# Kernel tuning notes

Measured on AMD Instinct MI355X. Metric: run time of the kernel, lower is better.

The kernel has to match this reference:

```python
import jax, jax.numpy as jnp
import numpy as np

B, N, D = 4, 2048, 1024  # in_features == out_features required by the original code path
SPARSITY = 0.01


def setup_inputs() -> dict:
    key = jax.random.key(0)
    k1, k2, k3 = jax.random.split(key, 3)
    x = jax.random.normal(k1, (B, N, D), dtype=jnp.float32)
    # Reproduce FrequencyLinearLayer.__init__: sparse top-k frequency weights.
    spatial = jax.random.normal(k2, (D, D), dtype=jnp.float32) * 0.02
    freq = jnp.fft.fft(spatial, axis=-1)  # complex64, (out, in) consumed as (D_in, D_out)
    k = int(D * SPARSITY)
    mag = jnp.abs(freq)
    kth = jax.lax.top_k(mag, k)[0][:, -1:]  # k-th largest magnitude per row
    w_sparse = jnp.where(mag >= kth, freq, 0.0 + 0.0j)
    bias = jax.random.normal(k3, (D,), dtype=jnp.float32) * 0.01
    return {
        "x": x,
        "w_freq_real": jnp.real(w_sparse).astype(jnp.float32),
        "w_freq_imag": jnp.imag(w_sparse).astype(jnp.float32),
        "bias": bias,
    }


def reference(x, w_freq_real, w_freq_imag, bias):
    # y = real(IFFT(FFT(x) @ W_freq)) + bias
    # The original materializes a (B,N,D_in,D_out) complex intermediate via
    # unsqueeze*multiply -> sum; that is exactly a complex matmul, expressed here as einsum.
    w = jax.lax.complex(w_freq_real, w_freq_imag)            # (D_in, D_out) complex64
    x_freq = jnp.fft.fft(x, axis=-1)                          # (B, N, D_in) complex64
    y_freq = jnp.einsum('bnd,do->bno', x_freq, w)             # (B, N, D_out)
    y = jnp.real(jnp.fft.ifft(y_freq, axis=-1))               # (B, N, D_out) float32
    return y + bias
```

## Files before the change

### kernel.cpp

```cpp
#include <hip/hip_runtime.h>
#include <hip/hip_bf16.h>
#include <math.h>

#define DD 1024
#define BT 8192
#define TWO_PI 6.28318530717958647692f

typedef float f32x4 __attribute__((ext_vector_type(4)));
typedef short bf16x8 __attribute__((ext_vector_type(8)));
typedef unsigned short u16x8 __attribute__((ext_vector_type(8)));
typedef unsigned short u16x4 __attribute__((ext_vector_type(4)));
typedef const __attribute__((address_space(1))) void g_void;
typedef __attribute__((address_space(3))) void l_void;

__device__ __forceinline__ unsigned short f2bf(float f) {
  unsigned int u = __float_as_uint(f);
  unsigned int r = (u + 0x7FFFu + ((u >> 16) & 1u)) >> 16;
  return (unsigned short)r;
}

__global__ __launch_bounds__(256) void transpose_W_kernel(
    const float* __restrict__ Wr, const float* __restrict__ Wi,
    float2* __restrict__ Wt) {
  __shared__ float tr[64][65];
  __shared__ float ti[64][65];
  const int k0 = blockIdx.y * 64, o0 = blockIdx.x * 64;
  for (int q = threadIdx.x; q < 64 * 64; q += 256) {
    int r = q >> 6, c = q & 63;
    tr[r][c] = Wr[(size_t)(k0 + r) * DD + o0 + c];
    ti[r][c] = Wi[(size_t)(k0 + r) * DD + o0 + c];
  }
  __syncthreads();
  for (int q = threadIdx.x; q < 64 * 64; q += 256) {
    int r = q >> 6, c = q & 63;
    Wt[(size_t)(o0 + r) * DD + k0 + c] = make_float2(tr[c][r], ti[c][r]);
  }
}

__global__ __launch_bounds__(256) void build_T_kernel(
    const float2* __restrict__ Wt, float2* __restrict__ T) {
  __shared__ float2 tw[DD];
  __shared__ int    kidx[DD];
  __shared__ float2 wval[DD];
  __shared__ int    offs[257];
  const int o = blockIdx.x, tid = threadIdx.x;

  for (int j = tid; j < DD; j += 256) {
    float s, c;
    sincosf((TWO_PI / DD) * (float)j, &s, &c);
    tw[j] = make_float2(c, s);
  }
  int cnt = 0;
  for (int k = tid; k < DD; k += 256) {
    float2 w = Wt[(size_t)o * DD + k];
    if (w.x != 0.f || w.y != 0.f) cnt++;
  }
  offs[tid + 1] = cnt;
  __syncthreads();
  if (tid == 0) {
    offs[0] = 0;
    for (int i = 1; i <= 256; i++) offs[i] += offs[i - 1];
  }
  __syncthreads();
  int p = offs[tid];
  for (int k = tid; k < DD; k += 256) {
    float2 w = Wt[(size_t)o * DD + k];
    if (w.x != 0.f || w.y != 0.f) { kidx[p] = k; wval[p] = w; p++; }
  }
  __syncthreads();
  const int nnz = offs[256];
  for (int d = tid; d < DD; d += 256) {
    float re = 0.f, im = 0.f;
    for (int j = 0; j < nnz; j++) {
      int    k  = kidx[j];
      float2 w  = wval[j];
      float2 cs = tw[(k * d) & (DD - 1)];
      re += w.x * cs.x + w.y * cs.y;
      im += w.y * cs.x - w.x * cs.y;
    }
    T[(size_t)o * DD + d] = make_float2(re, im);
  }
}

__global__ __launch_bounds__(256) void transpose_T_kernel(
    const float2* __restrict__ T, unsigned short* __restrict__ TT) {
  __shared__ float2 tile[64][65];
  const int o0 = blockIdx.x * 64, d0 = blockIdx.y * 64;
  for (int q = threadIdx.x; q < 64 * 64; q += 256) {
    int r = q >> 6, c = q & 63;
    tile[r][c] = T[(size_t)(o0 + r) * DD + d0 + c];
  }
  __syncthreads();
  for (int q = threadIdx.x; q < 64 * 64; q += 256) {
    int r = q >> 6, c = q & 63;
    float2 v = tile[c][r];
    TT[(size_t)(d0 + r) * 2048 + o0 + c]        = f2bf(v.x);
    TT[(size_t)(d0 + r) * 2048 + 1024 + o0 + c] = f2bf(v.y);
  }
}

__global__ __launch_bounds__(256) void gen_CS_kernel(unsigned short* __restrict__ CS) {
  int idx = blockIdx.x * 256 + threadIdx.x;
  int m = idx >> 10, o = idx & 1023;
  float s, c;
  sincosf((TWO_PI / DD) * (float)((m * o) & (DD - 1)), &s, &c);
  CS[(size_t)m * 2048 + o]        = f2bf(c);
  CS[(size_t)m * 2048 + 1024 + o] = f2bf(-s);
}

__global__ __launch_bounds__(256) void convert_x_kernel(
    const float* __restrict__ X, unsigned short* __restrict__ Xb) {
  size_t i = (size_t)blockIdx.x * 256 + threadIdx.x;
  const float4* p = (const float4*)(X + i * 8);
  float4 a = p[0], b = p[1];
  u16x8 v;
  v[0] = f2bf(a.x); v[1] = f2bf(a.y); v[2] = f2bf(a.z); v[3] = f2bf(a.w);
  v[4] = f2bf(b.x); v[5] = f2bf(b.y); v[6] = f2bf(b.z); v[7] = f2bf(b.w);
  *(u16x8*)(Xb + i * 8) = v;
}

template <int LDK, int MODE>
__global__ __launch_bounds__(256) void mfma_nt_kernel(
    const unsigned short* __restrict__ A,
    const unsigned short* __restrict__ B,
    const float* __restrict__ bias,
    float* __restrict__ Out, float scale, int ldo, int kLen) {
  __shared__ __align__(16) unsigned short Asm[128 * 32];
  __shared__ __align__(16) unsigned short Bsm[128 * 32];
  const int tid  = threadIdx.x;
  const int wave = tid >> 6, lane = tid & 63;
  const int wr = wave >> 1, wc = wave & 1;
  const int row0 = blockIdx.y * 128;
  const int col0 = blockIdx.x * 128;
  const int kBeg = blockIdx.z * kLen;

  f32x4 acc[4][4] = {};

  for (int k0 = kBeg; k0 < kBeg + kLen; k0 += 32) {
    __syncthreads();
#pragma unroll
    for (int is = 0; is < 2; is++) {
      int e = is * 256 + tid;
      int r = e >> 2, c = (e & 3) * 8;
      const unsigned short* ga = A + (size_t)(row0 + r) * LDK + k0 + c;
      const unsigned short* gb = B + (size_t)(col0 + r) * LDK + k0 + c;
      __builtin_amdgcn_global_load_lds((g_void*)ga, (l_void*)(Asm + is * 2048 + wave * 512), 16, 0, 0);
      __builtin_amdgcn_global_load_lds((g_void*)gb, (l_void*)(Bsm + is * 2048 + wave * 512), 16, 0, 0);
    }
    __syncthreads();

    bf16x8 af[4], bfr[4];
#pragma unroll
    for (int i = 0; i < 4; i++) {
      int ra = wr * 64 + i * 16 + (lane & 15);
      af[i]  = *(const bf16x8*)&Asm[ra * 32 + (lane >> 4) * 8];
      int rb = wc * 64 + i * 16 + (lane & 15);
      bfr[i] = *(const bf16x8*)&Bsm[rb * 32 + (lane >> 4) * 8];
    }
#pragma unroll
    for (int i = 0; i < 4; i++)
#pragma unroll
      for (int j = 0; j < 4; j++)
        acc[i][j] = __builtin_amdgcn_mfma_f32_16x16x32_bf16(af[i], bfr[j], acc[i][j], 0, 0, 0);
  }

  const int crow0 = row0 + wr * 64;
  const int ccol0 = col0 + wc * 64;
  if (MODE == 2) {
    float* O = Out + (size_t)blockIdx.z * DD * DD;
#pragma unroll
    for (int i = 0; i < 4; i++)
#pragma unroll
      for (int j = 0; j < 4; j++) {
        int cc = ccol0 + j * 16 + (lane & 15);
#pragma unroll
        for (int v = 0; v < 4; v++) {
          int rr = crow0 + i * 16 + (lane >> 4) * 4 + v;
          O[(size_t)rr * ldo + cc] = acc[i][j][v];
        }
      }
  } else {
    float bv[4];
#pragma unroll
    for (int j = 0; j < 4; j++)
      bv[j] = bias[ccol0 + j * 16 + (lane & 15)];
#pragma unroll
    for (int i = 0; i < 4; i++)
#pragma unroll
      for (int j = 0; j < 4; j++) {
        int cc = ccol0 + j * 16 + (lane & 15);
#pragma unroll
        for (int v = 0; v < 4; v++) {
          int rr = crow0 + i * 16 + (lane >> 4) * 4 + v;
          Out[(size_t)rr * ldo + cc] = acc[i][j][v] * scale + bv[j];
        }
      }
  }
}

__global__ __launch_bounds__(256) void reduce_M_kernel(
    const float* __restrict__ P, unsigned short* __restrict__ Mb) {
  const size_t NE = (size_t)DD * DD;
  size_t i = ((size_t)blockIdx.x * 256 + threadIdx.x) * 4;
  float4 s = *(const float4*)(P + i);
#pragma unroll
  for (int z = 1; z < 4; z++) {
    float4 p = *(const float4*)(P + z * NE + i);
    s.x += p.x; s.y += p.y; s.z += p.z; s.w += p.w;
  }
  const float inv = 1.0f / (float)DD;
  u16x4 v;
  v[0] = f2bf(s.x * inv); v[1] = f2bf(s.y * inv);
  v[2] = f2bf(s.z * inv); v[3] = f2bf(s.w * inv);
  *(u16x4*)(Mb + i) = v;
}

extern "C" void kernel_launch(void* const* d_in, const int* in_sizes, int n_in,
                              void* d_out, int out_size, void* d_ws, size_t ws_size,
                              hipStream_t stream) {
  const float* x    = (const float*)d_in[0];
  const float* wrp  = (const float*)d_in[1];
  const float* wip  = (const float*)d_in[2];
  const float* bias = (const float*)d_in[3];
  float*       y    = (float*)d_out;

  char* ws = (char*)d_ws;
  const size_t MB = 1024 * 1024;
  float2*         Wt = (float2*)(ws + 0);
  float2*         T  = (float2*)(ws + 8  * MB);
  unsigned short* TT = (unsigned short*)(ws + 16 * MB);
  unsigned short* CS = (unsigned short*)(ws + 20 * MB);
  unsigned short* Mb = (unsigned short*)(ws + 24 * MB);
  float*          P  = (float*)(ws + 0);
  unsigned short* Xb = (unsigned short*)(ws + 0);

  transpose_W_kernel<<<dim3(16, 16), 256, 0, stream>>>(wrp, wip, Wt);
  build_T_kernel<<<DD, 256, 0, stream>>>(Wt, T);
  transpose_T_kernel<<<dim3(16, 16), 256, 0, stream>>>(T, TT);
  gen_CS_kernel<<<4096, 256, 0, stream>>>(CS);
  mfma_nt_kernel<2048, 2><<<dim3(8, 8, 4), 256, 0, stream>>>(
      CS, TT, nullptr, P, 1.0f, DD, 512);
  reduce_M_kernel<<<DD * DD / (256 * 4), 256, 0, stream>>>(P, Mb);
  convert_x_kernel<<<4096, 256, 0, stream>>>(x, Xb);
  mfma_nt_kernel<1024, 0><<<dim3(8, 64, 1), 256, 0, stream>>>(
      Xb, Mb, bias, y, 1.0f, DD, 1024);
}
```

Measured before the change: 99.48 us.

## Deepen GEMM K-step, remap blocks across XCDs, parallelize sparse-index scan

The GEMM kernel now loads two 32-wide K slices per barrier pair, halving the number of synchronizations per tile, and uses a 1D grid with a swizzle that spreads consecutive tiles over the eight XCDs for better L2 locality. build_T replaces the serial single-thread prefix sum and double global read with register-held nonzeros and a parallel Hillis-Steele scan, shrinking shared index buffers to 64 entries. LDS use per GEMM block doubles, and the scan assumes at most 4 nonzeros per thread and 64 per row.

Result: slower. 106.6 us (+7.2%).

```diff
diff --git a/kernel.cpp b/kernel.cpp
--- a/kernel.cpp
+++ b/kernel.cpp
@@ -40,9 +40,9 @@
 __global__ __launch_bounds__(256) void build_T_kernel(
     const float2* __restrict__ Wt, float2* __restrict__ T) {
   __shared__ float2 tw[DD];
-  __shared__ int    kidx[DD];
-  __shared__ float2 wval[DD];
-  __shared__ int    offs[257];
+  __shared__ int    kidx[64];
+  __shared__ float2 wval[64];
+  __shared__ int    sc[256];
   const int o = blockIdx.x, tid = threadIdx.x;
 
   for (int j = tid; j < DD; j += 256) {
@@ -51,24 +51,27 @@
     tw[j] = make_float2(c, s);
   }
   int cnt = 0;
-  for (int k = tid; k < DD; k += 256) {
+  float2 wl[4];
+  int    kl[4];
+#pragma unroll
+  for (int q = 0; q < 4; q++) {
+    int k = tid + q * 256;
     float2 w = Wt[(size_t)o * DD + k];
-    if (w.x != 0.f || w.y != 0.f) cnt++;
-  }
-  offs[tid + 1] = cnt;
-  __syncthreads();
-  if (tid == 0) {
-    offs[0] = 0;
-    for (int i = 1; i <= 256; i++) offs[i] += offs[i - 1];
-  }
-  __syncthreads();
-  int p = offs[tid];
-  for (int k = tid; k < DD; k += 256) {
-    float2 w = Wt[(size_t)o * DD + k];
-    if (w.x != 0.f || w.y != 0.f) { kidx[p] = k; wval[p] = w; p++; }
-  }
-  __syncthreads();
-  const int nnz = offs[256];
+    if (w.x != 0.f || w.y != 0.f) { wl[cnt] = w; kl[cnt] = k; cnt++; }
+  }
+  sc[tid] = cnt;
+  __syncthreads();
+#pragma unroll
+  for (int dstep = 1; dstep < 256; dstep <<= 1) {
+    int v = (tid >= dstep) ? sc[tid - dstep] : 0;
+    __syncthreads();
+    sc[tid] += v;
+    __syncthreads();
+  }
+  int p = sc[tid] - cnt;
+  for (int q = 0; q < cnt; q++) { kidx[p + q] = kl[q]; wval[p + q] = wl[q]; }
+  __syncthreads();
+  const int nnz = sc[255];
   for (int d = tid; d < DD; d += 256) {
     float re = 0.f, im = 0.f;
     for (int j = 0; j < nnz; j++) {
@@ -119,55 +122,70 @@
   *(u16x8*)(Xb + i * 8) = v;
 }
 
-template <int LDK, int MODE>
+template <int LDK, int MODE, int GX>
 __global__ __launch_bounds__(256) void mfma_nt_kernel(
     const unsigned short* __restrict__ A,
     const unsigned short* __restrict__ B,
     const float* __restrict__ bias,
     float* __restrict__ Out, float scale, int ldo, int kLen) {
-  __shared__ __align__(16) unsigned short Asm[128 * 32];
-  __shared__ __align__(16) unsigned short Bsm[128 * 32];
+  __shared__ __align__(16) unsigned short Asm[2][128 * 32];
+  __shared__ __align__(16) unsigned short Bsm[2][128 * 32];
   const int tid  = threadIdx.x;
   const int wave = tid >> 6, lane = tid & 63;
   const int wr = wave >> 1, wc = wave & 1;
-  const int row0 = blockIdx.y * 128;
-  const int col0 = blockIdx.x * 128;
-  const int kBeg = blockIdx.z * kLen;
+
+  const int L     = blockIdx.x;
+  const int chunk = gridDim.x >> 3;
+  const int W     = (L & 7) * chunk + (L >> 3);
+  const int tx    = W % GX;
+  const int tyz   = W / GX;
+  const int ty    = (MODE == 2) ? (tyz & 7) : tyz;
+  const int tz    = (MODE == 2) ? (tyz >> 3) : 0;
+
+  const int row0 = ty * 128;
+  const int col0 = tx * 128;
+  const int kBeg = tz * kLen;
 
   f32x4 acc[4][4] = {};
 
-  for (int k0 = kBeg; k0 < kBeg + kLen; k0 += 32) {
-    __syncthreads();
-#pragma unroll
-    for (int is = 0; is < 2; is++) {
-      int e = is * 256 + tid;
-      int r = e >> 2, c = (e & 3) * 8;
-      const unsigned short* ga = A + (size_t)(row0 + r) * LDK + k0 + c;
-      const unsigned short* gb = B + (size_t)(col0 + r) * LDK + k0 + c;
-      __builtin_amdgcn_global_load_lds((g_void*)ga, (l_void*)(Asm + is * 2048 + wave * 512), 16, 0, 0);
-      __builtin_amdgcn_global_load_lds((g_void*)gb, (l_void*)(Bsm + is * 2048 + wave * 512), 16, 0, 0);
+  for (int k0 = kBeg; k0 < kBeg + kLen; k0 += 64) {
+    __syncthreads();
+#pragma unroll
+    for (int h = 0; h < 2; h++) {
+#pragma unroll
+      for (int is = 0; is < 2; is++) {
+        int e = is * 256 + tid;
+        int r = e >> 2, c = (e & 3) * 8;
+        const unsigned short* ga = A + (size_t)(row0 + r) * LDK + k0 + h * 32 + c;
+        const unsigned short* gb = B + (size_t)(col0 + r) * LDK + k0 + h * 32 + c;
+        __builtin_amdgcn_global_load_lds((g_void*)ga, (l_void*)(Asm[h] + is * 2048 + wave * 512), 16, 0, 0);
+        __builtin_amdgcn_global_load_lds((g_void*)gb, (l_void*)(Bsm[h] + is * 2048 + wave * 512), 16, 0, 0);
+      }
     }
     __syncthreads();
 
-    bf16x8 af[4], bfr[4];
-#pragma unroll
-    for (int i = 0; i < 4; i++) {
-      int ra = wr * 64 + i * 16 + (lane & 15);
-      af[i]  = *(const bf16x8*)&Asm[ra * 32 + (lane >> 4) * 8];
-      int rb = wc * 64 + i * 16 + (lane & 15);
-      bfr[i] = *(const bf16x8*)&Bsm[rb * 32 + (lane >> 4) * 8];
+#pragma unroll
+    for (int h = 0; h < 2; h++) {
+      bf16x8 af[4], bfr[4];
+#pragma unroll
+      for (int i = 0; i < 4; i++) {
+        int ra = wr * 64 + i * 16 + (lane & 15);
+        af[i]  = *(const bf16x8*)&Asm[h][ra * 32 + (lane >> 4) * 8];
+        int rb = wc * 64 + i * 16 + (lane & 15);
+        bfr[i] = *(const bf16x8*)&Bsm[h][rb * 32 + (lane >> 4) * 8];
+      }
+#pragma unroll
+      for (int i = 0; i < 4; i++)
+#pragma unroll
+        for (int j = 0; j < 4; j++)
+          acc[i][j] = __builtin_amdgcn_mfma_f32_16x16x32_bf16(af[i], bfr[j], acc[i][j], 0, 0, 0);
     }
-#pragma unroll
-    for (int i = 0; i < 4; i++)
-#pragma unroll
-      for (int j = 0; j < 4; j++)
-        acc[i][j] = __builtin_amdgcn_mfma_f32_16x16x32_bf16(af[i], bfr[j], acc[i][j], 0, 0, 0);
   }
 
   const int crow0 = row0 + wr * 64;
   const int ccol0 = col0 + wc * 64;
   if (MODE == 2) {
-    float* O = Out + (size_t)blockIdx.z * DD * DD;
+    float* O = Out + (size_t)tz * DD * DD;
 #pragma unroll
     for (int i = 0; i < 4; i++)
 #pragma unroll
@@ -238,10 +256,10 @@
   build_T_kernel<<<DD, 256, 0, stream>>>(Wt, T);
   transpose_T_kernel<<<dim3(16, 16), 256, 0, stream>>>(T, TT);
   gen_CS_kernel<<<4096, 256, 0, stream>>>(CS);
-  mfma_nt_kernel<2048, 2><<<dim3(8, 8, 4), 256, 0, stream>>>(
+  mfma_nt_kernel<2048, 2, 8><<<256, 256, 0, stream>>>(
       CS, TT, nullptr, P, 1.0f, DD, 512);
   reduce_M_kernel<<<DD * DD / (256 * 4), 256, 0, stream>>>(P, Mb);
   convert_x_kernel<<<4096, 256, 0, stream>>>(x, Xb);
-  mfma_nt_kernel<1024, 0><<<dim3(8, 64, 1), 256, 0, stream>>>(
+  mfma_nt_kernel<1024, 0, 8><<<512, 256, 0, stream>>>(
       Xb, Mb, bias, y, 1.0f, DD, 1024);
 }
```

## Double-buffer final GEMM with swizzled LDS and parallelize nnz compaction scan

Applied to the files above, without the earlier changes.

The final X·M GEMM is replaced by a dedicated kernel that uses a BK of 64, double-buffers its LDS tiles so the next tile's global loads overlap the current tile's MFMAs, and XOR-swizzles the LDS layout to reduce bank conflicts. build_T's serial single-thread prefix sum becomes a parallel Hillis-Steele scan, and nonzeros are kept in registers so W is read once. The scan assumes at most 4 nonzeros per thread and 64 per row, which holds for 1% sparsity but would overflow for denser weights.

New measurement: 102.0 us. 2.5% more time.

```diff
diff --git a/kernel.cpp b/kernel.cpp
--- a/kernel.cpp
+++ b/kernel.cpp
@@ -40,9 +40,9 @@
 __global__ __launch_bounds__(256) void build_T_kernel(
     const float2* __restrict__ Wt, float2* __restrict__ T) {
   __shared__ float2 tw[DD];
-  __shared__ int    kidx[DD];
-  __shared__ float2 wval[DD];
-  __shared__ int    offs[257];
+  __shared__ int    kidx[64];
+  __shared__ float2 wval[64];
+  __shared__ int    sc[256];
   const int o = blockIdx.x, tid = threadIdx.x;
 
   for (int j = tid; j < DD; j += 256) {
@@ -51,24 +51,27 @@
     tw[j] = make_float2(c, s);
   }
   int cnt = 0;
-  for (int k = tid; k < DD; k += 256) {
+  float2 wl[4];
+  int    kl[4];
+#pragma unroll
+  for (int q = 0; q < 4; q++) {
+    int k = tid + q * 256;
     float2 w = Wt[(size_t)o * DD + k];
-    if (w.x != 0.f || w.y != 0.f) cnt++;
-  }
-  offs[tid + 1] = cnt;
-  __syncthreads();
-  if (tid == 0) {
-    offs[0] = 0;
-    for (int i = 1; i <= 256; i++) offs[i] += offs[i - 1];
-  }
-  __syncthreads();
-  int p = offs[tid];
-  for (int k = tid; k < DD; k += 256) {
-    float2 w = Wt[(size_t)o * DD + k];
-    if (w.x != 0.f || w.y != 0.f) { kidx[p] = k; wval[p] = w; p++; }
-  }
-  __syncthreads();
-  const int nnz = offs[256];
+    if (w.x != 0.f || w.y != 0.f) { wl[cnt] = w; kl[cnt] = k; cnt++; }
+  }
+  sc[tid] = cnt;
+  __syncthreads();
+#pragma unroll
+  for (int dstep = 1; dstep < 256; dstep <<= 1) {
+    int v = (tid >= dstep) ? sc[tid - dstep] : 0;
+    __syncthreads();
+    sc[tid] += v;
+    __syncthreads();
+  }
+  int p = sc[tid] - cnt;
+  for (int q = 0; q < cnt; q++) { kidx[p + q] = kl[q]; wval[p + q] = wl[q]; }
+  __syncthreads();
+  const int nnz = sc[255];
   for (int d = tid; d < DD; d += 256) {
     float re = 0.f, im = 0.f;
     for (int j = 0; j < nnz; j++) {
@@ -215,6 +218,85 @@
   *(u16x4*)(Mb + i) = v;
 }
 
+__global__ __launch_bounds__(256) void gemm_y_kernel(
+    const unsigned short* __restrict__ Xb,
+    const unsigned short* __restrict__ Mb,
+    const float* __restrict__ bias,
+    float* __restrict__ Y) {
+  __shared__ __align__(16) unsigned short Asm[2][128 * 64];
+  __shared__ __align__(16) unsigned short Bsm[2][128 * 64];
+  const int tid  = threadIdx.x;
+  const int wave = tid >> 6, lane = tid & 63;
+  const int wr = wave >> 1, wc = wave & 1;
+  const int row0 = blockIdx.y * 128;
+  const int col0 = blockIdx.x * 128;
+
+#define STAGE(buf, kk)                                                        \
+  {                                                                           \
+    _Pragma("unroll")                                                         \
+    for (int p = 0; p < 4; p++) {                                             \
+      int e  = p * 256 + tid;                                                 \
+      int r  = e >> 3;                                                        \
+      int cs = ((e & 7) ^ ((e >> 3) & 7)) * 8;                                \
+      const unsigned short* ga = Xb + (size_t)(row0 + r) * DD + (kk) + cs;    \
+      const unsigned short* gb = Mb + (size_t)(col0 + r) * DD + (kk) + cs;    \
+      __builtin_amdgcn_global_load_lds((g_void*)ga,                           \
+          (l_void*)(Asm[buf] + p * 2048 + wave * 512), 16, 0, 0);             \
+      __builtin_amdgcn_global_load_lds((g_void*)gb,                           \
+          (l_void*)(Bsm[buf] + p * 2048 + wave * 512), 16, 0, 0);             \
+    }                                                                         \
+  }
+
+  f32x4 acc[4][4] = {};
+
+  STAGE(0, 0);
+  __syncthreads();
+
+  for (int t = 0; t < 16; ++t) {
+    const int cur = t & 1;
+    if (t < 15) STAGE(cur ^ 1, (t + 1) * 64);
+
+#pragma unroll
+    for (int half = 0; half < 2; half++) {
+      bf16x8 af[4], bfr[4];
+#pragma unroll
+      for (int i = 0; i < 4; i++) {
+        int ra = wr * 64 + i * 16 + (lane & 15);
+        int ca = ((half * 4 + (lane >> 4)) ^ (ra & 7)) * 8;
+        af[i]  = *(const bf16x8*)&Asm[cur][ra * 64 + ca];
+        int rb = wc * 64 + i * 16 + (lane & 15);
+        int cb = ((half * 4 + (lane >> 4)) ^ (rb & 7)) * 8;
+        bfr[i] = *(const bf16x8*)&Bsm[cur][rb * 64 + cb];
+      }
+#pragma unroll
+      for (int i = 0; i < 4; i++)
+#pragma unroll
+        for (int j = 0; j < 4; j++)
+          acc[i][j] = __builtin_amdgcn_mfma_f32_16x16x32_bf16(af[i], bfr[j], acc[i][j], 0, 0, 0);
+    }
+    __syncthreads();
+  }
+#undef STAGE
+
+  const int crow0 = row0 + wr * 64;
+  const int ccol0 = col0 + wc * 64;
+  float bv[4];
+#pragma unroll
+  for (int j = 0; j < 4; j++)
+    bv[j] = bias[ccol0 + j * 16 + (lane & 15)];
+#pragma unroll
+  for (int i = 0; i < 4; i++)
+#pragma unroll
+    for (int j = 0; j < 4; j++) {
+      int cc = ccol0 + j * 16 + (lane & 15);
+#pragma unroll
+      for (int v = 0; v < 4; v++) {
+        int rr = crow0 + i * 16 + (lane >> 4) * 4 + v;
+        Y[(size_t)rr * DD + cc] = acc[i][j][v] + bv[j];
+      }
+    }
+}
+
 extern "C" void kernel_launch(void* const* d_in, const int* in_sizes, int n_in,
                               void* d_out, int out_size, void* d_ws, size_t ws_size,
                               hipStream_t stream) {
@@ -242,6 +324,5 @@
       CS, TT, nullptr, P, 1.0f, DD, 512);
   reduce_M_kernel<<<DD * DD / (256 * 4), 256, 0, stream>>>(P, Mb);
   convert_x_kernel<<<4096, 256, 0, stream>>>(x, Xb);
-  mfma_nt_kernel<1024, 0><<<dim3(8, 64, 1), 256, 0, stream>>>(
-      Xb, Mb, bias, y, 1.0f, DD, 1024);
-}
+  gemm_y_kernel<<<dim3(8, 64), 256, 0, stream>>>(Xb, Mb, bias, y);
+}
```
